# Kernel optimization log

Hardware: AMD Instinct MI355X
Metric: run time of the kernel (lower is better)

Reference implementation:

```python
import jax, jax.numpy as jnp
import numpy as np

N, E = 50000, 400000
HID, HT = 128, 128
HEADS, C = 4, 128  # TransformerConv heads=4, out_channels=hidden_X


def setup_inputs() -> dict:
    key = jax.random.key(0)
    ks = jax.random.split(key, 16)
    s = lambda k, shape, fan: jax.random.normal(k, shape, jnp.float32) / np.sqrt(fan)
    return {
        "edge_index": jax.random.randint(ks[0], (2, E), 0, N, dtype=jnp.int32),
        "h_X": jax.random.normal(ks[1], (N, HID), jnp.float32),
        "h_t": jax.random.normal(ks[2], (1, HT), jnp.float32),
        # TransformerConv params: lin_query/key/value: (HID -> HEADS*C), lin_skip: (HID -> C)
        "Wq": s(ks[3], (HID, HEADS * C), HID), "bq": jnp.zeros((HEADS * C,), jnp.float32),
        "Wk": s(ks[4], (HID, HEADS * C), HID), "bk": jnp.zeros((HEADS * C,), jnp.float32),
        "Wv": s(ks[5], (HID, HEADS * C), HID), "bv": jnp.zeros((HEADS * C,), jnp.float32),
        "Wskip": s(ks[6], (HID, C), HID), "bskip": jnp.zeros((C,), jnp.float32),
        # update_X: Linear(HID+HT -> HID), LayerNorm(HID)
        "Wup": s(ks[7], (HID + HT, HID), HID + HT), "bup": jnp.zeros((HID,), jnp.float32),
        "gamma": jnp.ones((HID,), jnp.float32), "beta": jnp.zeros((HID,), jnp.float32),
    }


def transformer_conv(h_X, edge_index, Wq, bq, Wk, bk, Wv, bv, Wskip, bskip):
    n = h_X.shape[0]
    src, dst = edge_index[0], edge_index[1]  # messages flow src -> dst
    q = (h_X @ Wq + bq).reshape(n, HEADS, C)
    k = (h_X @ Wk + bk).reshape(n, HEADS, C)
    v = (h_X @ Wv + bv).reshape(n, HEADS, C)
    # per-edge attention scores [E, H]
    score = jnp.einsum('ehc,ehc->eh', q[dst], k[src]) / np.sqrt(C)
    # segment softmax over incoming edges of each destination node
    m = jax.ops.segment_max(score, dst, num_segments=n)          # [N, H]
    ex = jnp.exp(score - m[dst])                                 # [E, H]
    denom = jax.ops.segment_sum(ex, dst, num_segments=n)        # [N, H]
    alpha = ex / denom[dst]                                      # [E, H]
    agg = jax.ops.segment_sum(alpha[..., None] * v[src], dst, num_segments=n)  # [N, H, C]
    out = agg.mean(axis=1)                                       # concat=False -> mean over heads
    return out + h_X @ Wskip + bskip                             # root_weight=True


def reference(edge_index, h_X, h_t, Wq, bq, Wk, bk, Wv, bv, Wskip, bskip,
              Wup, bup, gamma, beta):
    n = h_X.shape[0]
    h_att = transformer_conv(h_X, edge_index, Wq, bq, Wk, bk, Wv, bv, Wskip, bskip)
    h_t_exp = jnp.broadcast_to(h_t, (n, h_t.shape[1]))
    h = jnp.concatenate([h_att, h_t_exp], axis=1)
    h = jax.nn.relu(h @ Wup + bup)
    # LayerNorm (eps=1e-5); Dropout is identity in eval
    mu = h.mean(axis=-1, keepdims=True)
    var = ((h - mu) ** 2).mean(axis=-1, keepdims=True)
    return (h - mu) / jnp.sqrt(var + 1e-5) * gamma + beta
```

## Files before the change

### kernel.cpp

```cpp
#include <hip/hip_runtime.h>

typedef unsigned short u16;
typedef unsigned int   u32;

#define HID   128
#define HEADS 4
#define CH    128
#define HC    512
#define UT    32

typedef __bf16 bf16x8v __attribute__((ext_vector_type(8)));
typedef float  f32x4v  __attribute__((ext_vector_type(4)));
union FragU { uint4 u; bf16x8v b; };

static __device__ __forceinline__ float bf2f(u16 u) {
  union { u32 u; float f; } x;
  x.u = ((u32)u) << 16;
  return x.f;
}
static __device__ __forceinline__ u16 f2bf(float f) {
  union { float f; u32 u; } x;
  x.f = f;
  u32 r = x.u + 0x7fffu + ((x.u >> 16) & 1u);
  return (u16)(r >> 16);
}

static __device__ __forceinline__ void unpack8(uint4 raw, float* dst) {
  dst[0] = bf2f((u16)(raw.x & 0xffffu));
  dst[1] = bf2f((u16)(raw.x >> 16));
  dst[2] = bf2f((u16)(raw.y & 0xffffu));
  dst[3] = bf2f((u16)(raw.y >> 16));
  dst[4] = bf2f((u16)(raw.z & 0xffffu));
  dst[5] = bf2f((u16)(raw.z >> 16));
  dst[6] = bf2f((u16)(raw.w & 0xffffu));
  dst[7] = bf2f((u16)(raw.w >> 16));
}

__global__ void zero_kernel(int* p, int n) {
  int i = blockIdx.x * 256 + threadIdx.x;
  if (i < n) p[i] = 0;
}

__global__ void hist_kernel(const int* dst_idx, int* deg, int E) {
  int e = blockIdx.x * 256 + threadIdx.x;
  if (e < E) atomicAdd(&deg[dst_idx[e]], 1);
}

__global__ void blocksum_kernel(const int* deg, int* bsums, int n) {
  __shared__ int buf[256];
  int i = blockIdx.x * 256 + threadIdx.x;
  int v = 0;
  if (i < n) v = deg[i];
  buf[threadIdx.x] = v;
  __syncthreads();
  for (int off = 128; off > 0; off >>= 1) {
    if (threadIdx.x < off) buf[threadIdx.x] += buf[threadIdx.x + off];
    __syncthreads();
  }
  if (threadIdx.x == 0) bsums[blockIdx.x] = buf[0];
}

__global__ void scanb_kernel(const int* bsums, int* boffs, int nb) {
  __shared__ int buf[256];
  __shared__ int carry_s;
  int tid = threadIdx.x;
  if (tid == 0) carry_s = 0;
  __syncthreads();
  for (int base = 0; base < nb; base += 256) {
    int i = base + tid;
    int v = 0;
    if (i < nb) v = bsums[i];
    buf[tid] = v;
    __syncthreads();
    for (int off = 1; off < 256; off <<= 1) {
      int t = 0;
      if (tid >= off) t = buf[tid - off];
      __syncthreads();
      buf[tid] += t;
      __syncthreads();
    }
    int incl = buf[tid] + carry_s;
    if (i < nb) boffs[i] = incl - v;
    __syncthreads();
    if (tid == 255) carry_s = incl;
    __syncthreads();
  }
}

__global__ void scanfinal_kernel(const int* deg, const int* boffs,
                                 int* row_ptr, int* cursor, int n) {
  __shared__ int buf[256];
  int tid = threadIdx.x;
  int i = blockIdx.x * 256 + tid;
  int v = 0;
  if (i < n) v = deg[i];
  buf[tid] = v;
  __syncthreads();
  for (int off = 1; off < 256; off <<= 1) {
    int t = 0;
    if (tid >= off) t = buf[tid - off];
    __syncthreads();
    buf[tid] += t;
    __syncthreads();
  }
  int incl = buf[tid] + boffs[blockIdx.x];
  if (i < n) {
    row_ptr[i + 1] = incl;
    cursor[i] = incl - v;
  }
  if (i == 0) row_ptr[0] = 0;
}

__global__ void scatter_kernel(const int* src_idx, const int* dst_idx,
                               int* cursor, int* col, int E) {
  int e = blockIdx.x * 256 + threadIdx.x;
  if (e < E) {
    int pos = atomicAdd(&cursor[dst_idx[e]], 1);
    col[pos] = src_idx[e];
  }
}

__global__ void packH_kernel(const float* __restrict__ hX,
                             u16* __restrict__ hpack, int N, int total) {
  int i = blockIdx.x * 256 + threadIdx.x;
  if (i >= total) return;
  int j = i & 7;
  int lane = (i >> 3) & 63;
  int kc = (i >> 9) & 3;
  int ntile = i >> 11;
  int node = ntile * 16 + (lane & 15);
  int k = kc * 32 + (lane >> 4) * 8 + j;
  float v = (node < N) ? hX[(size_t)node * HID + k] : 0.f;
  hpack[i] = f2bf(v);
}

__global__ void packW4_kernel(const float* __restrict__ Wq,
                              const float* __restrict__ Wk,
                              const float* __restrict__ Wv,
                              const float* __restrict__ Wsk,
                              u16* __restrict__ Wp, int total) {
  int i = blockIdx.x * 256 + threadIdx.x;
  if (i >= total) return;
  int j = i & 7;
  int lane = (i >> 3) & 63;
  int kc = (i >> 9) & 3;
  int ct = i >> 11;
  int n = ct * 16 + (lane & 15);
  int k = kc * 32 + (lane >> 4) * 8 + j;
  float w;
  if (n < 512) w = Wq[(size_t)k * HC + n];
  else if (n < 1024) w = Wk[(size_t)k * HC + (n - 512)];
  else if (n < 1536) w = Wv[(size_t)k * HC + (n - 1024)];
  else w = Wsk[(size_t)k * HID + (n - 1536)];
  Wp[i] = f2bf(w);
}

__global__ __launch_bounds__(256) void mfma_proj_kernel(
    const u16* __restrict__ hpack, const u16* __restrict__ Wp,
    const float* __restrict__ bq, const float* __restrict__ bk,
    const float* __restrict__ bv, const float* __restrict__ bsk,
    u16* __restrict__ qb, u16* __restrict__ kbuf, u16* __restrict__ vbuf,
    float* __restrict__ skipf, int N) {
  int t = threadIdx.x;
  int wv = t >> 6;
  int L = t & 63;
  int bx = blockIdx.x;
  int my0 = blockIdx.y * 8;

  FragU Bf[2][4];
  const u16* wb0 = Wp + (size_t)(bx * 8 + wv * 2) * 2048;
#pragma unroll
  for (int cc = 0; cc < 2; ++cc)
#pragma unroll
    for (int kc = 0; kc < 4; ++kc)
      Bf[cc][kc].u = *(const uint4*)(wb0 + cc * 2048 + kc * 512 + L * 8);

  int colq = L & 15;
  int quad = L >> 4;
  u16* outB_[2];
  float bval[2];
  int nl_[2];
  int isF32_[2];
#pragma unroll
  for (int cc = 0; cc < 2; ++cc) {
    int n = (bx * 8 + wv * 2 + cc) * 16 + colq;
    const float* bias;
    if (n < 512) {
      outB_[cc] = qb; bias = bq; nl_[cc] = n; isF32_[cc] = 0;
    } else if (n < 1024) {
      outB_[cc] = kbuf; bias = bk; nl_[cc] = n - 512; isF32_[cc] = 0;
    } else if (n < 1536) {
      outB_[cc] = vbuf; bias = bv; nl_[cc] = n - 1024; isF32_[cc] = 0;
    } else {
      outB_[cc] = (u16*)skipf; bias = bsk; nl_[cc] = n - 1536; isF32_[cc] = 1;
    }
    bval[cc] = bias[nl_[cc]];
  }

  const u16* ha = hpack + (size_t)my0 * 2048;

  for (int mt = 0; mt < 8; mt += 2) {
    FragU a0[4], a1[4];
#pragma unroll
    for (int kc = 0; kc < 4; ++kc) {
      a0[kc].u = *(const uint4*)(ha + (size_t)mt * 2048 + kc * 512 + L * 8);
      a1[kc].u =
          *(const uint4*)(ha + (size_t)(mt + 1) * 2048 + kc * 512 + L * 8);
    }

    f32x4v ac00 = (f32x4v){0.f, 0.f, 0.f, 0.f};
    f32x4v ac01 = (f32x4v){0.f, 0.f, 0.f, 0.f};
    f32x4v ac10 = (f32x4v){0.f, 0.f, 0.f, 0.f};
    f32x4v ac11 = (f32x4v){0.f, 0.f, 0.f, 0.f};
#pragma unroll
    for (int kc = 0; kc < 4; ++kc) {
      ac00 = __builtin_amdgcn_mfma_f32_16x16x32_bf16(a0[kc].b, Bf[0][kc].b,
                                                     ac00, 0, 0, 0);
      ac01 = __builtin_amdgcn_mfma_f32_16x16x32_bf16(a0[kc].b, Bf[1][kc].b,
                                                     ac01, 0, 0, 0);
      ac10 = __builtin_amdgcn_mfma_f32_16x16x32_bf16(a1[kc].b, Bf[0][kc].b,
                                                     ac10, 0, 0, 0);
      ac11 = __builtin_amdgcn_mfma_f32_16x16x32_bf16(a1[kc].b, Bf[1][kc].b,
                                                     ac11, 0, 0, 0);
    }

#pragma unroll
    for (int half = 0; half < 2; ++half) {
      int nodeBase = (my0 + mt + half) * 16 + quad * 4;
#pragma unroll
      for (int cc = 0; cc < 2; ++cc) {
        const f32x4v& a =
            half ? (cc ? ac11 : ac10) : (cc ? ac01 : ac00);
        if (isF32_[cc]) {
#pragma unroll
          for (int rg = 0; rg < 4; ++rg) {
            int node = nodeBase + rg;
            if (node < N)
              skipf[(size_t)node * HID + nl_[cc]] = a[rg] + bval[cc];
          }
        } else {
          u16* ob = outB_[cc];
#pragma unroll
          for (int rg = 0; rg < 4; ++rg) {
            int node = nodeBase + rg;
            if (node < N)
              ob[(size_t)node * HC + nl_[cc]] = f2bf(a[rg] + bval[cc]);
          }
        }
      }
    }
  }
}

__global__ void fused_attn_kernel(const u16* __restrict__ qb,
                                  const u16* __restrict__ kb,
                                  const u16* __restrict__ vb,
                                  const int* __restrict__ row_ptr,
                                  const int* __restrict__ col_src,
                                  float* out, int N) {
  int node = blockIdx.x * 4 + (threadIdx.x >> 6);
  if (node >= N) return;
  int lane = threadIdx.x & 63;
  int head = lane >> 4;
  int r = lane & 15;
  int foff = head * CH + r * 8;
  const float sscale = 0.08838834764831845f;

  float qf[8];
  unpack8(*(const uint4*)(qb + (size_t)node * HC + foff), qf);

  float m = -3.402823466e38f;
  float l = 0.f;
  float acc[8];
  for (int j = 0; j < 8; ++j) acc[j] = 0.f;

  int e0 = row_ptr[node];
  int e1 = row_ptr[node + 1];
  int e = e0;

  for (; e + 4 <= e1; e += 4) {
    int s0 = col_src[e];
    int s1 = col_src[e + 1];
    int s2 = col_src[e + 2];
    int s3 = col_src[e + 3];
    uint4 k0 = *(const uint4*)(kb + (size_t)s0 * HC + foff);
    uint4 k1 = *(const uint4*)(kb + (size_t)s1 * HC + foff);
    uint4 k2 = *(const uint4*)(kb + (size_t)s2 * HC + foff);
    uint4 k3 = *(const uint4*)(kb + (size_t)s3 * HC + foff);
    uint4 v0 = *(const uint4*)(vb + (size_t)s0 * HC + foff);
    uint4 v1 = *(const uint4*)(vb + (size_t)s1 * HC + foff);
    uint4 v2 = *(const uint4*)(vb + (size_t)s2 * HC + foff);
    uint4 v3 = *(const uint4*)(vb + (size_t)s3 * HC + foff);

    float kf0[8], kf1[8], kf2[8], kf3[8];
    unpack8(k0, kf0);
    unpack8(k1, kf1);
    unpack8(k2, kf2);
    unpack8(k3, kf3);
    float p0 = 0.f, p1 = 0.f, p2 = 0.f, p3 = 0.f;
    for (int j = 0; j < 8; ++j) {
      p0 = fmaf(kf0[j], qf[j], p0);
      p1 = fmaf(kf1[j], qf[j], p1);
      p2 = fmaf(kf2[j], qf[j], p2);
      p3 = fmaf(kf3[j], qf[j], p3);
    }
    p0 += __shfl_xor(p0, 1);
    p1 += __shfl_xor(p1, 1);
    p2 += __shfl_xor(p2, 1);
    p3 += __shfl_xor(p3, 1);
    p0 += __shfl_xor(p0, 2);
    p1 += __shfl_xor(p1, 2);
    p2 += __shfl_xor(p2, 2);
    p3 += __shfl_xor(p3, 2);
    p0 += __shfl_xor(p0, 4);
    p1 += __shfl_xor(p1, 4);
    p2 += __shfl_xor(p2, 4);
    p3 += __shfl_xor(p3, 4);
    p0 += __shfl_xor(p0, 8);
    p1 += __shfl_xor(p1, 8);
    p2 += __shfl_xor(p2, 8);
    p3 += __shfl_xor(p3, 8);
    float sc0 = p0 * sscale;
    float sc1 = p1 * sscale;
    float sc2 = p2 * sscale;
    float sc3 = p3 * sscale;
    float mnew = fmaxf(fmaxf(m, fmaxf(sc0, sc1)), fmaxf(sc2, sc3));
    float so = __expf(m - mnew);
    float pe0 = __expf(sc0 - mnew);
    float pe1 = __expf(sc1 - mnew);
    float pe2 = __expf(sc2 - mnew);
    float pe3 = __expf(sc3 - mnew);
    l = l * so + (pe0 + pe1) + (pe2 + pe3);
    float vf0[8], vf1[8], vf2[8], vf3[8];
    unpack8(v0, vf0);
    unpack8(v1, vf1);
    unpack8(v2, vf2);
    unpack8(v3, vf3);
    for (int j = 0; j < 8; ++j) {
      float add = fmaf(pe0, vf0[j],
                       fmaf(pe1, vf1[j], fmaf(pe2, vf2[j], pe3 * vf3[j])));
      acc[j] = fmaf(acc[j], so, add);
    }
    m = mnew;
  }

  for (; e < e1; ++e) {
    int s0 = col_src[e];
    uint4 k0 = *(const uint4*)(kb + (size_t)s0 * HC + foff);
    uint4 v0 = *(const uint4*)(vb + (size_t)s0 * HC + foff);
    float kf0[8];
    unpack8(k0, kf0);
    float p0 = 0.f;
    for (int j = 0; j < 8; ++j) p0 = fmaf(kf0[j], qf[j], p0);
    p0 += __shfl_xor(p0, 1);
    p0 += __shfl_xor(p0, 2);
    p0 += __shfl_xor(p0, 4);
    p0 += __shfl_xor(p0, 8);
    float sc0 = p0 * sscale;
    float mnew = fmaxf(m, sc0);
    float so = __expf(m - mnew);
    float pe0 = __expf(sc0 - mnew);
    l = l * so + pe0;
    float vf0[8];
    unpack8(v0, vf0);
    for (int j = 0; j < 8; ++j) acc[j] = fmaf(acc[j], so, pe0 * vf0[j]);
    m = mnew;
  }

  float inv = 0.f;
  if (l > 0.f) inv = 1.0f / l;
  float val[8];
  for (int j = 0; j < 8; ++j) {
    float x = acc[j] * inv;
    x += __shfl_xor(x, 16);
    x += __shfl_xor(x, 32);
    val[j] = x * 0.25f;
  }

  if (head == 0) {
    float* p = out + (size_t)node * HID + r * 8;
    float4 a = *(const float4*)(p);
    float4 b = *(const float4*)(p + 4);
    a.x += val[0]; a.y += val[1]; a.z += val[2]; a.w += val[3];
    b.x += val[4]; b.y += val[5]; b.z += val[6]; b.w += val[7];
    *(float4*)(p) = a;
    *(float4*)(p + 4) = b;
  }
}

__global__ void cvec_kernel(const float* h_t, const float* Wup,
                            const float* bup, float* cvec) {
  __shared__ float part[4][128];
  int c = threadIdx.x & 127;
  int kc = threadIdx.x >> 7;
  float acc = 0.f;
  for (int k = kc * 32; k < kc * 32 + 32; ++k)
    acc = fmaf(h_t[k], Wup[(size_t)(128 + k) * 128 + c], acc);
  part[kc][c] = acc;
  __syncthreads();
  if (kc == 0)
    cvec[c] = part[0][c] + part[1][c] + part[2][c] + part[3][c] + bup[c];
}

__global__ __launch_bounds__(256) void ATTLayer_19396072308956_kernel(
    float* out, const float* __restrict__ Wup, const float* __restrict__ cvec,
    const float* __restrict__ gamma, const float* __restrict__ beta, int N) {
  __shared__ float Wl[64 * 128];
  __shared__ float Hl[UT * 128];
  int t = threadIdx.x;
  int n0 = blockIdx.x * UT;

  for (int i = t * 4; i < UT * 128; i += 1024) {
    int node = n0 + (i >> 7);
    float4 v;
    if (node < N) {
      v = *(const float4*)(out + (size_t)node * HID + (i & 127));
    } else {
      v.x = 0.f; v.y = 0.f; v.z = 0.f; v.w = 0.f;
    }
    *(float4*)(Hl + i) = v;
  }

  int wv = t >> 6;
  int r = t & 63;
  int c0 = 2 * r;
  float2 cv = *(const float2*)(cvec + c0);
  float a0[8];
  float a1[8];
  for (int j = 0; j < 8; ++j) {
    a0[j] = cv.x;
    a1[j] = cv.y;
  }

  for (int ph = 0; ph < 2; ++ph) {
    __syncthreads();
    for (int i = t * 4; i < 64 * 128; i += 1024) {
      *(float4*)(Wl + i) = *(const float4*)(Wup + (size_t)ph * 64 * 128 + i);
    }
    __syncthreads();
    const float* hbase = Hl + (wv * 8) * 128 + ph * 64;
#pragma unroll 8
    for (int k = 0; k < 64; ++k) {
      float2 w2 = *(const float2*)(Wl + k * 128 + c0);
      for (int j = 0; j < 8; ++j) {
        float h = hbase[j * 128 + k];
        a0[j] = fmaf(h, w2.x, a0[j]);
        a1[j] = fmaf(h, w2.y, a1[j]);
      }
    }
  }

  float2 g = *(const float2*)(gamma + c0);
  float2 b = *(const float2*)(beta + c0);
  for (int j = 0; j < 8; ++j) {
    int node = n0 + wv * 8 + j;
    float r0 = fmaxf(a0[j], 0.f);
    float r1 = fmaxf(a1[j], 0.f);
    float s = r0 + r1;
    for (int msk = 1; msk < 64; msk <<= 1) s += __shfl_xor(s, msk);
    float mean = s * (1.0f / 128.0f);
    float d0 = r0 - mean;
    float d1 = r1 - mean;
    float sq = d0 * d0 + d1 * d1;
    for (int msk = 1; msk < 64; msk <<= 1) sq += __shfl_xor(sq, msk);
    float rstd = rsqrtf(sq * (1.0f / 128.0f) + 1e-5f);
    if (node < N) {
      float2 o;
      o.x = d0 * rstd * g.x + b.x;
      o.y = d1 * rstd * g.y + b.y;
      *(float2*)(out + (size_t)node * HID + c0) = o;
    }
  }
}

extern "C" void kernel_launch(void* const* d_in, const int* in_sizes, int n_in,
                              void* d_out, int out_size, void* d_ws,
                              size_t ws_size, hipStream_t stream) {
  (void)n_in;
  (void)out_size;
  (void)ws_size;

  const int* edge_index = (const int*)d_in[0];
  const float* hX    = (const float*)d_in[1];
  const float* h_t   = (const float*)d_in[2];
  const float* Wq    = (const float*)d_in[3];
  const float* bq    = (const float*)d_in[4];
  const float* Wk    = (const float*)d_in[5];
  const float* bk    = (const float*)d_in[6];
  const float* Wv    = (const float*)d_in[7];
  const float* bv    = (const float*)d_in[8];
  const float* Wskip = (const float*)d_in[9];
  const float* bskip = (const float*)d_in[10];
  const float* Wup   = (const float*)d_in[11];
  const float* bup   = (const float*)d_in[12];
  const float* gamma = (const float*)d_in[13];
  const float* beta  = (const float*)d_in[14];

  const int E = in_sizes[0] / 2;
  const int N = in_sizes[1] / HID;
  const int* src_idx = edge_index;
  const int* dst_idx = edge_index + E;
  const int NB = (N + 255) / 256;
  const int NTILES = (N + 15) / 16;
  const int NTILES8 = ((NTILES + 7) / 8) * 8;

  char* w = (char*)d_ws;
  size_t off = 0;
  float* cvec = (float*)(w + off);
  off += 256 * 4;
  int* deg = (int*)(w + off);
  off += ((size_t)N * 4 + 255) / 256 * 256;
  int* row_ptr = (int*)(w + off);
  off += ((size_t)(N + 1) * 4 + 255) / 256 * 256;
  int* cursor = (int*)(w + off);
  off += ((size_t)N * 4 + 255) / 256 * 256;
  int* bsums = (int*)(w + off);
  off += ((size_t)NB * 4 + 255) / 256 * 256;
  int* boffs = (int*)(w + off);
  off += ((size_t)NB * 4 + 255) / 256 * 256;
  int* col = (int*)(w + off);
  off += ((size_t)E * 4 + 255) / 256 * 256;
  u16* hpack = (u16*)(w + off);
  off += ((size_t)NTILES8 * 2048 * 2 + 255) / 256 * 256;
  u16* Wp = (u16*)(w + off);
  off += ((size_t)128 * 1664 * 2 + 255) / 256 * 256;
  u16* bigA = (u16*)(w + off);
  off += ((size_t)N * HC * 2 + 255) / 256 * 256;
  u16* bigB = (u16*)(w + off);
  off += ((size_t)N * HC * 2 + 255) / 256 * 256;
  u16* bigC = (u16*)(w + off);
  off += ((size_t)N * HC * 2 + 255) / 256 * 256;

  float* out = (float*)d_out;

  zero_kernel<<<NB, 256, 0, stream>>>(deg, N);
  hist_kernel<<<(E + 255) / 256, 256, 0, stream>>>(dst_idx, deg, E);
  blocksum_kernel<<<NB, 256, 0, stream>>>(deg, bsums, N);
  scanb_kernel<<<1, 256, 0, stream>>>(bsums, boffs, NB);
  scanfinal_kernel<<<NB, 256, 0, stream>>>(deg, boffs, row_ptr, cursor, N);
  scatter_kernel<<<(E + 255) / 256, 256, 0, stream>>>(src_idx, dst_idx, cursor,
                                                      col, E);

  int totH = NTILES8 * 2048;
  packH_kernel<<<(totH + 255) / 256, 256, 0, stream>>>(hX, hpack, N, totH);
  packW4_kernel<<<(128 * 1664 + 255) / 256, 256, 0, stream>>>(
      Wq, Wk, Wv, Wskip, Wp, 128 * 1664);

  cvec_kernel<<<1, 512, 0, stream>>>(h_t, Wup, bup, cvec);

  mfma_proj_kernel<<<dim3(13, NTILES8 / 8), 256, 0, stream>>>(
      hpack, Wp, bq, bk, bv, bskip, bigA, bigB, bigC, out, N);

  fused_attn_kernel<<<(N + 3) / 4, 256, 0, stream>>>(bigA, bigB, bigC, row_ptr,
                                                     col, out, N);

  ATTLayer_19396072308956_kernel<<<(N + UT - 1) / UT, 256, 0, stream>>>(
      out, Wup, cvec, gamma, beta, N);
}
```

Before: 394.5 us.

## Software-pipeline K/V gathers in fused attention and hoist skip-output load

The fused attention loop now prefetches the next group of four source nodes' K and V vectors into registers while the current group is processed, hiding gather latency. The skip-connection output row is loaded at kernel start instead of at the end, and explicit unroll pragmas are added. The degree-zeroing kernel is replaced by hipMemsetAsync. The prefetch doubles the registers held for K/V, which may reduce occupancy.

```diff
diff --git a/kernel.cpp b/kernel.cpp
--- a/kernel.cpp
+++ b/kernel.cpp
@@ -34,11 +34,6 @@
   dst[5] = bf2f((u16)(raw.z >> 16));
   dst[6] = bf2f((u16)(raw.w & 0xffffu));
   dst[7] = bf2f((u16)(raw.w >> 16));
-}
-
-__global__ void zero_kernel(int* p, int n) {
-  int i = blockIdx.x * 256 + threadIdx.x;
-  if (i < n) p[i] = 0;
 }
 
 __global__ void hist_kernel(const int* dst_idx, int* deg, int E) {
@@ -269,35 +264,66 @@
   float qf[8];
   unpack8(*(const uint4*)(qb + (size_t)node * HC + foff), qf);
 
+  float* orow = out + (size_t)node * HID + r * 8;
+  float4 oa = {0.f, 0.f, 0.f, 0.f};
+  float4 obv = {0.f, 0.f, 0.f, 0.f};
+  if (head == 0) {
+    oa = *(const float4*)(orow);
+    obv = *(const float4*)(orow + 4);
+  }
+
   float m = -3.402823466e38f;
   float l = 0.f;
   float acc[8];
+#pragma unroll
   for (int j = 0; j < 8; ++j) acc[j] = 0.f;
 
   int e0 = row_ptr[node];
   int e1 = row_ptr[node + 1];
-  int e = e0;
-
-  for (; e + 4 <= e1; e += 4) {
-    int s0 = col_src[e];
-    int s1 = col_src[e + 1];
-    int s2 = col_src[e + 2];
-    int s3 = col_src[e + 3];
-    uint4 k0 = *(const uint4*)(kb + (size_t)s0 * HC + foff);
-    uint4 k1 = *(const uint4*)(kb + (size_t)s1 * HC + foff);
-    uint4 k2 = *(const uint4*)(kb + (size_t)s2 * HC + foff);
-    uint4 k3 = *(const uint4*)(kb + (size_t)s3 * HC + foff);
-    uint4 v0 = *(const uint4*)(vb + (size_t)s0 * HC + foff);
-    uint4 v1 = *(const uint4*)(vb + (size_t)s1 * HC + foff);
-    uint4 v2 = *(const uint4*)(vb + (size_t)s2 * HC + foff);
-    uint4 v3 = *(const uint4*)(vb + (size_t)s3 * HC + foff);
+  int nfull = (e1 - e0) >> 2;
+
+  uint4 ck[4], cv[4];
+  if (nfull > 0) {
+    int s0 = col_src[e0];
+    int s1 = col_src[e0 + 1];
+    int s2 = col_src[e0 + 2];
+    int s3 = col_src[e0 + 3];
+    ck[0] = *(const uint4*)(kb + (size_t)s0 * HC + foff);
+    ck[1] = *(const uint4*)(kb + (size_t)s1 * HC + foff);
+    ck[2] = *(const uint4*)(kb + (size_t)s2 * HC + foff);
+    ck[3] = *(const uint4*)(kb + (size_t)s3 * HC + foff);
+    cv[0] = *(const uint4*)(vb + (size_t)s0 * HC + foff);
+    cv[1] = *(const uint4*)(vb + (size_t)s1 * HC + foff);
+    cv[2] = *(const uint4*)(vb + (size_t)s2 * HC + foff);
+    cv[3] = *(const uint4*)(vb + (size_t)s3 * HC + foff);
+  }
+
+  for (int g = 0; g < nfull; ++g) {
+    uint4 nk[4], nv[4];
+    int hasNext = (g + 1 < nfull);
+    if (hasNext) {
+      int nb = e0 + (g + 1) * 4;
+      int s0 = col_src[nb];
+      int s1 = col_src[nb + 1];
+      int s2 = col_src[nb + 2];
+      int s3 = col_src[nb + 3];
+      nk[0] = *(const uint4*)(kb + (size_t)s0 * HC + foff);
+      nk[1] = *(const uint4*)(kb + (size_t)s1 * HC + foff);
+      nk[2] = *(const uint4*)(kb + (size_t)s2 * HC + foff);
+      nk[3] = *(const uint4*)(kb + (size_t)s3 * HC + foff);
+      nv[0] = *(const uint4*)(vb + (size_t)s0 * HC + foff);
+      nv[1] = *(const uint4*)(vb + (size_t)s1 * HC + foff);
+      nv[2] = *(const uint4*)(vb + (size_t)s2 * HC + foff);
+      nv[3] = *(const uint4*)(vb + (size_t)s3 * HC + foff);
+    }
 
     float kf0[8], kf1[8], kf2[8], kf3[8];
-    unpack8(k0, kf0);
-    unpack8(k1, kf1);
-    unpack8(k2, kf2);
-    unpack8(k3, kf3);
+    unpack8(ck[0], kf0);
+    unpack8(ck[1], kf1);
+    unpack8(ck[2], kf2);
+    unpack8(ck[3], kf3);
     float p0 = 0.f, p1 = 0.f, p2 = 0.f, p3 = 0.f;
+#pragma unroll
     for (int j = 0; j < 8; ++j) {
       p0 = fmaf(kf0[j], qf[j], p0);
       p1 = fmaf(kf1[j], qf[j], p1);
@@ -332,25 +358,35 @@
     float pe3 = __expf(sc3 - mnew);
     l = l * so + (pe0 + pe1) + (pe2 + pe3);
     float vf0[8], vf1[8], vf2[8], vf3[8];
-    unpack8(v0, vf0);
-    unpack8(v1, vf1);
-    unpack8(v2, vf2);
-    unpack8(v3, vf3);
+    unpack8(cv[0], vf0);
+    unpack8(cv[1], vf1);
+    unpack8(cv[2], vf2);
+    unpack8(cv[3], vf3);
+#pragma unroll
     for (int j = 0; j < 8; ++j) {
       float add = fmaf(pe0, vf0[j],
                        fmaf(pe1, vf1[j], fmaf(pe2, vf2[j], pe3 * vf3[j])));
       acc[j] = fmaf(acc[j], so, add);
     }
     m = mnew;
-  }
-
-  for (; e < e1; ++e) {
+
+    if (hasNext) {
+#pragma unroll
+      for (int j = 0; j < 4; ++j) {
+        ck[j] = nk[j];
+        cv[j] = nv[j];
+      }
+    }
+  }
+
+  for (int e = e0 + nfull * 4; e < e1; ++e) {
     int s0 = col_src[e];
     uint4 k0 = *(const uint4*)(kb + (size_t)s0 * HC + foff);
     uint4 v0 = *(const uint4*)(vb + (size_t)s0 * HC + foff);
     float kf0[8];
     unpack8(k0, kf0);
     float p0 = 0.f;
+#pragma unroll
     for (int j = 0; j < 8; ++j) p0 = fmaf(kf0[j], qf[j], p0);
     p0 += __shfl_xor(p0, 1);
     p0 += __shfl_xor(p0, 2);
@@ -363,6 +399,7 @@
     l = l * so + pe0;
     float vf0[8];
     unpack8(v0, vf0);
+#pragma unroll
     for (int j = 0; j < 8; ++j) acc[j] = fmaf(acc[j], so, pe0 * vf0[j]);
     m = mnew;
   }
@@ -370,6 +407,7 @@
   float inv = 0.f;
   if (l > 0.f) inv = 1.0f / l;
   float val[8];
+#pragma unroll
   for (int j = 0; j < 8; ++j) {
     float x = acc[j] * inv;
     x += __shfl_xor(x, 16);
@@ -378,13 +416,16 @@
   }
 
   if (head == 0) {
-    float* p = out + (size_t)node * HID + r * 8;
-    float4 a = *(const float4*)(p);
-    float4 b = *(const float4*)(p + 4);
-    a.x += val[0]; a.y += val[1]; a.z += val[2]; a.w += val[3];
-    b.x += val[4]; b.y += val[5]; b.z += val[6]; b.w += val[7];
-    *(float4*)(p) = a;
-    *(float4*)(p + 4) = b;
+    oa.x += val[0];
+    oa.y += val[1];
+    oa.z += val[2];
+    oa.w += val[3];
+    obv.x += val[4];
+    obv.y += val[5];
+    obv.z += val[6];
+    obv.w += val[7];
+    *(float4*)(orow) = oa;
+    *(float4*)(orow + 4) = obv;
   }
 }
 
@@ -533,7 +574,7 @@
 
   float* out = (float*)d_out;
 
-  zero_kernel<<<NB, 256, 0, stream>>>(deg, N);
+  hipMemsetAsync(deg, 0, (size_t)N * 4, stream);
   hist_kernel<<<(E + 255) / 256, 256, 0, stream>>>(dst_idx, deg, E);
   blocksum_kernel<<<NB, 256, 0, stream>>>(deg, bsums, N);
   scanb_kernel<<<1, 256, 0, stream>>>(bsums, boffs, NB);
```

Measured after the change: 430.7 us. 1.09x slower.
